# Kernel optimization log

Hardware: AMD Instinct MI355X
Metric: run time of the kernel (lower is better)

The kernel has to match this reference:

```python
import jax, jax.numpy as jnp
import numpy as np
import math

B, S, HID, H = 4, 4096, 1024, 16
DH = HID // H  # 64

def setup_inputs() -> dict:
    key = jax.random.key(0)
    ks = jax.random.split(key, 6)
    query = jax.random.normal(ks[0], (B, S, HID), dtype=jnp.float32)
    key_t = jax.random.normal(ks[1], (B, S, HID), dtype=jnp.float32)
    value = jax.random.normal(ks[2], (B, S, HID), dtype=jnp.float32)
    attn_mask = jax.random.normal(ks[3], (B, S, H, H), dtype=jnp.float32)
    # nn.Linear(hidden, 3*hidden): weight (3H, H), bias (3H,)
    W_qkv = jax.random.normal(ks[4], (3 * HID, HID), dtype=jnp.float32) * (1.0 / math.sqrt(HID))
    b_qkv = jax.random.normal(ks[5], (3 * HID,), dtype=jnp.float32) * 0.01
    return {"query": query, "key": key_t, "value": value, "attn_mask": attn_mask,
            "W_qkv": W_qkv, "b_qkv": b_qkv}

def reference(query, key, value, attn_mask, W_qkv, b_qkv):
    # fused QKV projection (only `query` is used, matching the source)
    qkv = jnp.einsum('bsh,oh->bso', query, W_qkv) + b_qkv  # (B,S,3*HID)
    q, k, v = jnp.split(qkv, 3, axis=-1)
    q = q.reshape(B, S, H, DH)
    k = k.reshape(B, S, H, DH)
    v = v.reshape(B, S, H, DH)
    # NOTE: no (B,H,S,D) permute in the source -> scores are head-vs-head per position
    scale = 1.0 / math.sqrt(DH)
    qk = jnp.einsum('bshd,bsgd->bshg', q, k) * scale + attn_mask  # (B,S,H,H)
    attn_weight = jax.nn.softmax(qk, axis=-1)
    # dropout_p=0 (eval): identity
    o = jnp.einsum('bshg,bsgd->bshd', attn_weight, v)  # (B,S,H,DH)
    return o.reshape(B, S, HID)
```

## Files before the change

kernel.cpp:

```cpp
#include <hip/hip_runtime.h>
#include <cstdint>
#include <cstddef>


typedef __attribute__((ext_vector_type(8))) short bf16x8;
typedef __attribute__((ext_vector_type(4))) float f32x4;

__device__ inline unsigned short f2bf(float f) {
  unsigned int i = __float_as_uint(f);
  i += 0x7fff + ((i >> 16) & 1);
  return (unsigned short)(i >> 16);
}

__device__ inline void async16(const void* g, void* l) {
  __builtin_amdgcn_global_load_lds(
      (const __attribute__((address_space(1))) void*)g,
      (__attribute__((address_space(3))) void*)l, 16, 0, 0);
}

__device__ inline void unpack8(bf16x8 v, float* f) {
  union { bf16x8 s; unsigned int u[4]; } x; x.s = v;
  #pragma unroll
  for (int i = 0; i < 4; ++i) {
    f[2 * i]     = __uint_as_float(x.u[i] << 16);
    f[2 * i + 1] = __uint_as_float(x.u[i] & 0xffff0000u);
  }
}

__global__ __launch_bounds__(256) void cast_kernel(const float* __restrict__ in,
                                                   unsigned short* __restrict__ out,
                                                   int n) {
  int i = (blockIdx.x * 256 + threadIdx.x) * 4;
  if (i >= n) return;
  float4 v = *(const float4*)(in + i);
  union { unsigned short u[4]; unsigned long long ll; } o;
  o.u[0] = f2bf(v.x); o.u[1] = f2bf(v.y); o.u[2] = f2bf(v.z); o.u[3] = f2bf(v.w);
  *(unsigned long long*)(out + i) = o.ll;
}

#define GK 1024
#define GN 3072
__global__ __launch_bounds__(256) void gemm_qkv(const unsigned short* __restrict__ A,
                                                const unsigned short* __restrict__ Bm,
                                                const float* __restrict__ bias,
                                                unsigned short* __restrict__ C) {
  __shared__ unsigned short As[128 * 64];
  __shared__ unsigned short Bs[128 * 64];
  const int m0 = blockIdx.x * 128;
  const int n0 = blockIdx.y * 128;
  const int tid  = threadIdx.x;
  const int lane = tid & 63;
  const int wave = tid >> 6;
  const int wm = wave & 1, wn = wave >> 1;
  const int fr = lane & 15;
  const int fq = lane >> 4;

  f32x4 acc[4][4] = {};

  for (int k0 = 0; k0 < GK; k0 += 64) {
    #pragma unroll
    for (int t = 0; t < 4; ++t) {
      int sbase = t * 256 + wave * 64;
      int sl = sbase + lane;
      int r = sl >> 3;
      int c = ((sl & 7) ^ (r & 7)) * 8;
      async16(&A[(size_t)(m0 + r) * GK + k0 + c], &As[sbase * 8]);
      async16(&Bm[(size_t)(n0 + r) * GK + k0 + c], &Bs[sbase * 8]);
    }
    __syncthreads();
    #pragma unroll
    for (int ks = 0; ks < 64; ks += 32) {
      const int cbase = ks >> 3;
      bf16x8 af[4], bf[4];
      #pragma unroll
      for (int i = 0; i < 4; ++i) {
        int arow = wm * 64 + i * 16 + fr;
        int ac = (cbase + fq) ^ (arow & 7);
        af[i] = *(const bf16x8*)&As[arow * 64 + ac * 8];
        int brow = wn * 64 + i * 16 + fr;
        int bc = (cbase + fq) ^ (brow & 7);
        bf[i] = *(const bf16x8*)&Bs[brow * 64 + bc * 8];
      }
      #pragma unroll
      for (int i = 0; i < 4; ++i)
        #pragma unroll
        for (int j = 0; j < 4; ++j)
          acc[i][j] = __builtin_amdgcn_mfma_f32_16x16x32_bf16(af[i], bf[j], acc[i][j], 0, 0, 0);
    }
    __syncthreads();
  }

  #pragma unroll
  for (int i = 0; i < 4; ++i) {
    #pragma unroll
    for (int j = 0; j < 4; ++j) {
      int col = n0 + wn * 64 + j * 16 + fr;
      float bc = bias[col];
      #pragma unroll
      for (int r = 0; r < 4; ++r) {
        int row = m0 + wm * 64 + i * 16 + fq * 4 + r;
        C[(size_t)row * GN + col] = f2bf(acc[i][j][r] + bc);
      }
    }
  }
}

__global__ __launch_bounds__(256) void attn_kernel(const unsigned short* __restrict__ QKV,
                                                   const float* __restrict__ mask,
                                                   float* __restrict__ out) {
  __shared__ unsigned short shKV[4][2048];
  const int wave = threadIdx.x >> 6;
  const int lane = threadIdx.x & 63;
  const int pos = blockIdx.x * 4 + wave;

  const unsigned short* row = QKV + (size_t)pos * 3072;

  #pragma unroll
  for (int t = 0; t < 4; ++t)
    async16(&row[1024 + t * 512 + (size_t)lane * 8], &shKV[wave][t * 512]);

  bf16x8 q0 = *(const bf16x8*)&row[lane * 16];
  bf16x8 q1 = *(const bf16x8*)&row[lane * 16 + 8];

  const int h = lane >> 2;
  const int dg = lane & 3;

  const float* mrow = mask + (size_t)pos * 256 + h * 16;
  float4 m4[4];
  #pragma unroll
  for (int t = 0; t < 4; ++t) m4[t] = *(const float4*)&mrow[t * 4];

  float q[16];
  unpack8(q0, q);
  unpack8(q1, q + 8);

  asm volatile("s_waitcnt vmcnt(0)" ::: "memory");

  float s[16];
  #pragma unroll
  for (int g = 0; g < 16; ++g) {
    const unsigned short* kp = &shKV[wave][g * 64 + dg * 16];
    float kf[16];
    unpack8(*(const bf16x8*)kp, kf);
    unpack8(*(const bf16x8*)(kp + 8), kf + 8);
    float acc = 0.f;
    #pragma unroll
    for (int d = 0; d < 16; ++d) acc += q[d] * kf[d];
    s[g] = acc;
  }
  #pragma unroll
  for (int g = 0; g < 16; ++g) {
    s[g] += __shfl_xor(s[g], 1);
    s[g] += __shfl_xor(s[g], 2);
  }

  const float* mp = (const float*)m4;
  float mx = -1e30f;
  #pragma unroll
  for (int g = 0; g < 16; ++g) {
    s[g] = s[g] * 0.125f + mp[g];
    mx = fmaxf(mx, s[g]);
  }
  float sum = 0.f;
  #pragma unroll
  for (int g = 0; g < 16; ++g) { s[g] = __expf(s[g] - mx); sum += s[g]; }
  float inv = 1.f / sum;

  float o[16];
  #pragma unroll
  for (int dd = 0; dd < 16; ++dd) o[dd] = 0.f;
  #pragma unroll
  for (int g = 0; g < 16; ++g) {
    const unsigned short* vp = &shKV[wave][1024 + g * 64 + dg * 16];
    float vf[16];
    unpack8(*(const bf16x8*)vp, vf);
    unpack8(*(const bf16x8*)(vp + 8), vf + 8);
    float p = s[g];
    #pragma unroll
    for (int dd = 0; dd < 16; ++dd) o[dd] += p * vf[dd];
  }

  float* op = out + (size_t)pos * 1024 + lane * 16;
  #pragma unroll
  for (int t = 0; t < 4; ++t) {
    float4 w;
    w.x = o[t * 4 + 0] * inv; w.y = o[t * 4 + 1] * inv;
    w.z = o[t * 4 + 2] * inv; w.w = o[t * 4 + 3] * inv;
    *(float4*)(op + t * 4) = w;
  }
}

extern "C" void kernel_launch(void* const* d_in, const int* in_sizes, int n_in,
                              void* d_out, int out_size, void* d_ws, size_t ws_size,
                              hipStream_t stream) {
  const float* query = (const float*)d_in[0];
  const float* mask  = (const float*)d_in[3];
  const float* Wqkv  = (const float*)d_in[4];
  const float* bqkv  = (const float*)d_in[5];
  float* out = (float*)d_out;

  unsigned short* qb   = (unsigned short*)d_ws;
  unsigned short* wb   = (unsigned short*)((char*)d_ws + 33554432);
  unsigned short* qkvb = (unsigned short*)((char*)d_ws + 39845888);

  cast_kernel<<<16384, 256, 0, stream>>>(query, qb, 16777216);
  cast_kernel<<<3072, 256, 0, stream>>>(Wqkv, wb, 3145728);

  dim3 g(128, 24);
  gemm_qkv<<<g, 256, 0, stream>>>(qb, wb, bqkv, qkvb);

  attn_kernel<<<4096, 256, 0, stream>>>(qkvb, mask, out);
}
```

Baseline: 358.6 us.

## Rewrite QKV GEMM with 256x256 tiles, double-buffered async loads, and block swizzle

The QKV projection GEMM moves from 128x128 tiles with 256 threads and a single LDS buffer to 256x256 tiles with 512 threads. Global-to-LDS async loads are double-buffered and interleaved with MFMA phases, using explicit vmcnt waits, barriers, sched_barrier and setprio. The launch becomes a 1D grid whose block index is swizzled in groups of 8 to improve L2 reuse. The aim is to hide memory latency behind compute and raise data reuse per tile, at the cost of more LDS (128 KB per block) and higher register pressure.

```diff
diff --git a/kernel.cpp b/kernel.cpp
--- a/kernel.cpp
+++ b/kernel.cpp
@@ -40,67 +40,109 @@
 
 #define GK 1024
 #define GN 3072
-__global__ __launch_bounds__(256) void gemm_qkv(const unsigned short* __restrict__ A,
-                                                const unsigned short* __restrict__ Bm,
-                                                const float* __restrict__ bias,
-                                                unsigned short* __restrict__ C) {
-  __shared__ unsigned short As[128 * 64];
-  __shared__ unsigned short Bs[128 * 64];
-  const int m0 = blockIdx.x * 128;
-  const int n0 = blockIdx.y * 128;
+__global__ __launch_bounds__(512, 2) void gemm_qkv(const unsigned short* __restrict__ A,
+                                                   const unsigned short* __restrict__ Bm,
+                                                   const float* __restrict__ bias,
+                                                   unsigned short* __restrict__ C) {
+  __shared__ unsigned short As[2][256][64];
+  __shared__ unsigned short Bs[2][256][64];
+
+  const int bid = blockIdx.x;
+  const int swz = (bid & 7) * 96 + (bid >> 3);
+  const int m0 = (swz / 12) * 256;
+  const int n0 = (swz % 12) * 256;
+
   const int tid  = threadIdx.x;
   const int lane = tid & 63;
   const int wave = tid >> 6;
-  const int wm = wave & 1, wn = wave >> 1;
+  const int wm = wave & 1;
+  const int wn = wave >> 1;
   const int fr = lane & 15;
   const int fq = lane >> 4;
 
-  f32x4 acc[4][4] = {};
-
-  for (int k0 = 0; k0 < GK; k0 += 64) {
-    #pragma unroll
-    for (int t = 0; t < 4; ++t) {
-      int sbase = t * 256 + wave * 64;
-      int sl = sbase + lane;
-      int r = sl >> 3;
-      int c = ((sl & 7) ^ (r & 7)) * 8;
-      async16(&A[(size_t)(m0 + r) * GK + k0 + c], &As[sbase * 8]);
-      async16(&Bm[(size_t)(n0 + r) * GK + k0 + c], &Bs[sbase * 8]);
+  const int r0 = tid >> 3;
+  const int c0 = (tid & 7) ^ (r0 & 7);
+  const unsigned short* gA = A  + (size_t)(m0 + r0) * GK + c0 * 8;
+  const unsigned short* gB = Bm + (size_t)(n0 + r0) * GK + c0 * 8;
+  const int ls0 = wave * 512;
+
+#define STAGE_A(tt, hh) do {                                                   \
+    unsigned short* lb_ = &As[(tt) & 1][(hh) * 128][0];                        \
+    const unsigned short* g_ = gA + (size_t)(hh) * 128 * GK + (tt) * 64;       \
+    async16(g_, lb_ + ls0);                                                    \
+    async16(g_ + (size_t)64 * GK, lb_ + 4096 + ls0);                           \
+  } while (0)
+#define STAGE_B(tt, hh) do {                                                   \
+    unsigned short* lb_ = &Bs[(tt) & 1][(hh) * 128][0];                        \
+    const unsigned short* g_ = gB + (size_t)(hh) * 128 * GK + (tt) * 64;       \
+    async16(g_, lb_ + ls0);                                                    \
+    async16(g_ + (size_t)64 * GK, lb_ + 4096 + ls0);                           \
+  } while (0)
+
+  f32x4 acc[8][4] = {};
+
+  STAGE_A(0, 0); STAGE_A(0, 1); STAGE_B(0, 0); STAGE_B(0, 1);
+  STAGE_B(1, 0); STAGE_A(1, 0); STAGE_B(1, 1);
+
+  for (int t = 0; t < 16; ++t) {
+    const int cur = t & 1;
+    if (t < 15) { asm volatile("s_waitcnt vmcnt(6)" ::: "memory"); }
+    else        { asm volatile("s_waitcnt vmcnt(0)" ::: "memory"); }
+    __builtin_amdgcn_s_barrier();
+    __builtin_amdgcn_sched_barrier(0);
+
+    bf16x8 bfr[4][2];
+    #pragma unroll
+    for (int p = 0; p < 4; ++p) {
+      bf16x8 af[2][2];
+      #pragma unroll
+      for (int ii = 0; ii < 2; ++ii) {
+        const int rA = (p * 2 + ii) * 32 + wm * 16 + fr;
+        #pragma unroll
+        for (int ks = 0; ks < 2; ++ks)
+          af[ii][ks] = *(const bf16x8*)&As[cur][rA][((ks * 4 + fq) ^ (rA & 7)) * 8];
+      }
+      if (p == 0) {
+        #pragma unroll
+        for (int j = 0; j < 4; ++j) {
+          const int rB = wn * 64 + j * 16 + fr;
+          #pragma unroll
+          for (int ks = 0; ks < 2; ++ks)
+            bfr[j][ks] = *(const bf16x8*)&Bs[cur][rB][((ks * 4 + fq) ^ (rB & 7)) * 8];
+        }
+      }
+      if (p == 1 && t + 1 < 16) { STAGE_A(t + 1, 1); }
+      if (p == 2 && t + 2 < 16) { STAGE_B(t + 2, 0); }
+      if (p == 3 && t + 2 < 16) { STAGE_A(t + 2, 0); STAGE_B(t + 2, 1); }
+
+      __builtin_amdgcn_s_barrier();
+      __builtin_amdgcn_sched_barrier(0);
+      __builtin_amdgcn_s_setprio(1);
+      #pragma unroll
+      for (int ks = 0; ks < 2; ++ks)
+        #pragma unroll
+        for (int ii = 0; ii < 2; ++ii)
+          #pragma unroll
+          for (int j = 0; j < 4; ++j)
+            acc[p * 2 + ii][j] = __builtin_amdgcn_mfma_f32_16x16x32_bf16(
+                af[ii][ks], bfr[j][ks], acc[p * 2 + ii][j], 0, 0, 0);
+      __builtin_amdgcn_s_setprio(0);
+      __builtin_amdgcn_sched_barrier(0);
     }
-    __syncthreads();
-    #pragma unroll
-    for (int ks = 0; ks < 64; ks += 32) {
-      const int cbase = ks >> 3;
-      bf16x8 af[4], bf[4];
+  }
+#undef STAGE_A
+#undef STAGE_B
+
+  #pragma unroll
+  for (int j = 0; j < 4; ++j) {
+    const int col = n0 + wn * 64 + j * 16 + fr;
+    const float bc = bias[col];
+    #pragma unroll
+    for (int i = 0; i < 8; ++i) {
+      const int rowb = m0 + i * 32 + wm * 16 + fq * 4;
       #pragma unroll
-      for (int i = 0; i < 4; ++i) {
-        int arow = wm * 64 + i * 16 + fr;
-        int ac = (cbase + fq) ^ (arow & 7);
-        af[i] = *(const bf16x8*)&As[arow * 64 + ac * 8];
-        int brow = wn * 64 + i * 16 + fr;
-        int bc = (cbase + fq) ^ (brow & 7);
-        bf[i] = *(const bf16x8*)&Bs[brow * 64 + bc * 8];
-      }
-      #pragma unroll
-      for (int i = 0; i < 4; ++i)
-        #pragma unroll
-        for (int j = 0; j < 4; ++j)
-          acc[i][j] = __builtin_amdgcn_mfma_f32_16x16x32_bf16(af[i], bf[j], acc[i][j], 0, 0, 0);
-    }
-    __syncthreads();
-  }
-
-  #pragma unroll
-  for (int i = 0; i < 4; ++i) {
-    #pragma unroll
-    for (int j = 0; j < 4; ++j) {
-      int col = n0 + wn * 64 + j * 16 + fr;
-      float bc = bias[col];
-      #pragma unroll
-      for (int r = 0; r < 4; ++r) {
-        int row = m0 + wm * 64 + i * 16 + fq * 4 + r;
-        C[(size_t)row * GN + col] = f2bf(acc[i][j][r] + bc);
-      }
+      for (int rr = 0; rr < 4; ++rr)
+        C[(size_t)(rowb + rr) * GN + col] = f2bf(acc[i][j][rr] + bc);
     }
   }
 }
@@ -206,8 +248,7 @@
   cast_kernel<<<16384, 256, 0, stream>>>(query, qb, 16777216);
   cast_kernel<<<3072, 256, 0, stream>>>(Wqkv, wb, 3145728);
 
-  dim3 g(128, 24);
-  gemm_qkv<<<g, 256, 0, stream>>>(qb, wb, bqkv, qkvb);
+  gemm_qkv<<<768, 512, 0, stream>>>(qb, wb, bqkv, qkvb);
 
   attn_kernel<<<4096, 256, 0, stream>>>(qkvb, mask, out);
 }
```

After: 356.2 us. Within noise of the previous version (-0.7%).
